# Performance work log

Measured on AMD Instinct MI355X. Metric: run time of the kernel, lower is better.

## Reference

```python
import jax, jax.numpy as jnp
import numpy as np

EPS = 0.1
P, C, T_MLP, C_MLP, B = 196, 768, 384, 3072, 64


def yat(x, W, b, alpha):
    # x: (..., in), W: (out, in), b: (out,), alpha: (1,)
    dot_nb = jnp.einsum('...i,oi->...o', x, W)          # no-bias dot (shared GEMM)
    dot = dot_nb + b
    w_norm_sq = jnp.sum(W * W, axis=1)                   # (out,)
    x_norm_sq = jnp.sum(x * x, axis=-1, keepdims=True)   # (..., 1)
    dist_sq = w_norm_sq + x_norm_sq - 2.0 * dot_nb
    out_f = W.shape[0]
    scale_base = out_f / np.log(out_f + 1.0)
    scale = jnp.sqrt(jnp.asarray(scale_base, x.dtype)) ** alpha[0]
    return scale * (dot * dot) / (dist_sq + EPS)


def setup_inputs() -> dict:
    key = jax.random.key(0)
    ks = jax.random.split(key, 7)
    x = jax.random.normal(ks[0], (B, P, C), dtype=jnp.float32)
    # token-mixing YAT: in=P, out=T_MLP
    tw = jax.random.normal(ks[1], (T_MLP, P), dtype=jnp.float32) / np.sqrt(P)
    tb = jnp.zeros((T_MLP,), jnp.float32)
    t_alpha = jnp.ones((1,), jnp.float32)
    # token-mixing linear: T_MLP -> P
    w2 = jax.random.uniform(ks[2], (P, T_MLP), jnp.float32, -1, 1) / np.sqrt(T_MLP)
    b2 = jax.random.uniform(ks[3], (P,), jnp.float32, -1, 1) / np.sqrt(T_MLP)
    # channel-mixing YAT: in=C, out=C_MLP
    cw = jax.random.normal(ks[4], (C_MLP, C), dtype=jnp.float32) / np.sqrt(C)
    cb = jnp.zeros((C_MLP,), jnp.float32)
    c_alpha = jnp.ones((1,), jnp.float32)
    # channel-mixing linear: C_MLP -> C
    w4 = jax.random.uniform(ks[5], (C, C_MLP), jnp.float32, -1, 1) / np.sqrt(C_MLP)
    b4 = jax.random.uniform(ks[6], (C,), jnp.float32, -1, 1) / np.sqrt(C_MLP)
    return {"x": x, "tw": tw, "tb": tb, "t_alpha": t_alpha, "w2": w2, "b2": b2,
            "cw": cw, "cb": cb, "c_alpha": c_alpha, "w4": w4, "b4": b4}


def reference(x, tw, tb, t_alpha, w2, b2, cw, cb, c_alpha, w4, b4):
    # Token mixing (operates over patch dim)
    shortcut = x
    xt = jnp.swapaxes(x, 1, 2)                 # (B, C, P)
    h = yat(xt, tw, tb, t_alpha)               # (B, C, T_MLP)
    h = jnp.einsum('bct,pt->bcp', h, w2) + b2  # (B, C, P)
    x = shortcut + jnp.swapaxes(h, 1, 2)
    # Channel mixing (operates over hidden dim)
    shortcut = x
    h = yat(x, cw, cb, c_alpha)                # (B, P, C_MLP)
    h = jnp.einsum('bpm,cm->bpc', h, w4) + b4  # (B, P, C)
    return shortcut + h
```

## Files before the change

### kernel.cpp

```cpp
#include <hip/hip_runtime.h>
#include <hip/hip_bf16.h>
#include <math.h>

#define B_   64
#define P_   196
#define PPAD 224
#define C_   768
#define TM_  384
#define CM_  3072
#define EPSY 0.1f

typedef unsigned short u16;
typedef __attribute__((ext_vector_type(8))) short bf16x8;
typedef __attribute__((ext_vector_type(4))) float f32x4;

__device__ __forceinline__ float bf2f(u16 v) {
    return __uint_as_float(((unsigned int)v) << 16);
}
__device__ __forceinline__ u16 f2bf(float f) {
    unsigned int u = __float_as_uint(f);
    unsigned int rounding = 0x7FFFu + ((u >> 16) & 1u);
    return (u16)((u + rounding) >> 16);
}

__device__ __forceinline__ void gl_lds16(const u16* g, u16* l) {
    __builtin_amdgcn_global_load_lds(
        (const __attribute__((address_space(1))) unsigned int*)g,
        (__attribute__((address_space(3))) unsigned int*)l,
        16, 0, 0);
}


__global__ __launch_bounds__(256) void k_prep_xT(const float* __restrict__ x,
                                                 u16* __restrict__ xT,
                                                 float* __restrict__ xn1) {
    __shared__ u16 tile[32][33];
    __shared__ float colsum[32];
    const int b = blockIdx.z, p0 = blockIdx.x * 32, c0 = blockIdx.y * 32;
    const int tx = threadIdx.x & 31, ty = threadIdx.x >> 5;
    if (threadIdx.x < 32) colsum[threadIdx.x] = 0.f;
    const float* xb = x + (size_t)b * P_ * C_;
    float s = 0.f;
    #pragma unroll
    for (int r = 0; r < 4; ++r) {
        int p = p0 + ty + r * 8;
        float v = (p < P_) ? xb[(size_t)p * C_ + c0 + tx] : 0.f;
        u16 h = f2bf(v);
        tile[ty + r * 8][tx] = h;
        float vb = bf2f(h);
        s = fmaf(vb, vb, s);
    }
    __syncthreads();
    u16* dst = xT + ((size_t)b * C_ + c0) * PPAD + p0;
    #pragma unroll
    for (int r = 0; r < 4; ++r) {
        int cl = ty + r * 8;
        dst[(size_t)cl * PPAD + tx] = tile[tx][cl];
    }
    atomicAdd(&colsum[tx], s);
    __syncthreads();
    if (threadIdx.x < 32)
        atomicAdd(&xn1[(size_t)b * C_ + c0 + threadIdx.x], colsum[threadIdx.x]);
}

__device__ __forceinline__ void pad_norm_body(const float* in, u16* outb, float* norm,
                                              int rows, int inlen, int outlen,
                                              int bid, int tid) {
    int wave = (bid * 256 + tid) >> 6;
    int lane = tid & 63;
    if (wave >= rows) return;
    const float* src = in + (size_t)wave * inlen;
    u16* dst = outb + (size_t)wave * outlen;
    float s = 0.f;
    for (int i = lane; i < outlen; i += 64) {
        float v = (i < inlen) ? src[i] : 0.f;
        u16 h = f2bf(v);
        dst[i] = h;
        float vv = bf2f(h);
        s = fmaf(vv, vv, s);
    }
    #pragma unroll
    for (int off = 32; off > 0; off >>= 1) s += __shfl_down(s, off, 64);
    if (lane == 0) norm[wave] = s;
}

__global__ __launch_bounds__(256) void k_prep_weights(
    const float* __restrict__ tw, u16* __restrict__ twb, float* __restrict__ twn,
    const float* __restrict__ cw, u16* __restrict__ cwb, float* __restrict__ cwn,
    const float* __restrict__ w2, u16* __restrict__ w2b,
    const float* __restrict__ w4, u16* __restrict__ w4b) {
    int bid = blockIdx.x, tid = threadIdx.x;
    if (bid < 96) {
        pad_norm_body(tw, twb, twn, TM_, P_, PPAD, bid, tid);
    } else if (bid < 864) {
        pad_norm_body(cw, cwb, cwn, CM_, C_, C_, bid - 96, tid);
    } else if (bid < 1248) {
        int idx = (bid - 864) * 256 + tid;
        int row = idx / TM_;
        w2b[idx] = (row < P_) ? f2bf(w2[(size_t)row * TM_ + (idx % TM_)]) : (u16)0;
    } else {
        int idx = (bid - 1248) * 256 + tid;
        float4 v = ((const float4*)w4)[idx];
        ushort4 o;
        o.x = f2bf(v.x); o.y = f2bf(v.y); o.z = f2bf(v.z); o.w = f2bf(v.w);
        ((ushort4*)w4b)[idx] = o;
    }
}

__device__ __forceinline__ void mfma_mainloop(
    const u16* __restrict__ A, const u16* __restrict__ B,
    int lda, int ldb, int kiters,
    f32x4 (&acc)[4][4], u16* As, u16* Bs) {
    const int t = threadIdx.x;
    const int wid = t >> 6, lane = t & 63;
    const int quad = lane >> 4, l15 = lane & 15;
    const u16* Aw = As + (wid >> 1) * (64 * 32);
    const u16* Bw = Bs + (wid & 1) * (64 * 32);
    const int row0 = t >> 2, kc = (t & 3) * 8;
    const int row1 = 64 + row0;

    for (int it = 0; it < kiters; ++it) {
        int k0 = it * 32;
        gl_lds16(A + (size_t)row0 * lda + k0 + kc, As + wid * 512);
        gl_lds16(A + (size_t)row1 * lda + k0 + kc, As + 2048 + wid * 512);
        gl_lds16(B + (size_t)row0 * ldb + k0 + kc, Bs + wid * 512);
        gl_lds16(B + (size_t)row1 * ldb + k0 + kc, Bs + 2048 + wid * 512);
        __syncthreads();
        bf16x8 af[4], bfr[4];
        #pragma unroll
        for (int i = 0; i < 4; ++i)
            af[i] = *(const bf16x8*)(Aw + ((i * 16 + l15) * 32 + quad * 8));
        #pragma unroll
        for (int j = 0; j < 4; ++j)
            bfr[j] = *(const bf16x8*)(Bw + ((j * 16 + l15) * 32 + quad * 8));
        #pragma unroll
        for (int i = 0; i < 4; ++i)
            #pragma unroll
            for (int j = 0; j < 4; ++j)
                acc[i][j] = __builtin_amdgcn_mfma_f32_16x16x32_bf16(af[i], bfr[j], acc[i][j], 0, 0, 0);
        __syncthreads();
    }
}

#define MFMA_PROLOGUE(AP, BP, LDA, LDB, KITERS)                          \
    __shared__ u16 As[128 * 32];                                         \
    __shared__ u16 Bs[128 * 32];                                         \
    const int t = threadIdx.x;                                           \
    const int wid = t >> 6, lane = t & 63;                               \
    const int quad = lane >> 4, l15 = lane & 15;                         \
    const int m0 = blockIdx.x * 128, n0 = blockIdx.y * 128;              \
    f32x4 acc[4][4];                                                     \
    _Pragma("unroll")                                                    \
    for (int i = 0; i < 4; ++i)                                          \
        _Pragma("unroll")                                                \
        for (int j = 0; j < 4; ++j) acc[i][j] = (f32x4){0.f,0.f,0.f,0.f};\
    mfma_mainloop(AP, BP, LDA, LDB, KITERS, acc, As, Bs);                \
    const int rbase = m0 + (wid >> 1) * 64;                              \
    const int cbase = n0 + (wid & 1) * 64;

__global__ __launch_bounds__(256) void k1_token_yat(
    const u16* __restrict__ xT, const u16* __restrict__ twb,
    const float* __restrict__ tb, const float* __restrict__ twn,
    const float* __restrict__ xn1, const float* __restrict__ alpha, float sb,
    u16* __restrict__ h1) {
    MFMA_PROLOGUE(xT + (size_t)m0 * PPAD, twb + (size_t)n0 * PPAD, PPAD, PPAD, PPAD / 32)
    float scale = powf(sqrtf(sb), alpha[0]);
    #pragma unroll
    for (int i = 0; i < 4; ++i) {
        #pragma unroll
        for (int j = 0; j < 4; ++j) {
            int col = cbase + j * 16 + l15;
            float bn = tb[col], wnn = twn[col];
            #pragma unroll
            for (int reg = 0; reg < 4; ++reg) {
                int row = rbase + i * 16 + quad * 4 + reg;
                float dnb = acc[i][j][reg];
                float dot = dnb + bn;
                float dist = wnn + xn1[row] - 2.f * dnb;
                h1[(size_t)row * TM_ + col] = f2bf(scale * dot * dot / (dist + EPSY));
            }
        }
    }
}

__global__ __launch_bounds__(256) void k3_chan_yat(
    const u16* __restrict__ x1b, const u16* __restrict__ cwb,
    const float* __restrict__ cb, const float* __restrict__ cwn,
    const float* __restrict__ xn2, const float* __restrict__ alpha, float sb,
    u16* __restrict__ h3) {
    MFMA_PROLOGUE(x1b + (size_t)m0 * C_, cwb + (size_t)n0 * C_, C_, C_, C_ / 32)
    float scale = powf(sqrtf(sb), alpha[0]);
    #pragma unroll
    for (int i = 0; i < 4; ++i) {
        #pragma unroll
        for (int j = 0; j < 4; ++j) {
            int col = cbase + j * 16 + l15;
            float bn = cb[col], wnn = cwn[col];
            #pragma unroll
            for (int reg = 0; reg < 4; ++reg) {
                int row = rbase + i * 16 + quad * 4 + reg;
                float dnb = acc[i][j][reg];
                float dot = dnb + bn;
                float dist = wnn + xn2[row] - 2.f * dnb;
                h3[(size_t)row * CM_ + col] = f2bf(scale * dot * dot / (dist + EPSY));
            }
        }
    }
}

__global__ __launch_bounds__(256) void k2_token_out(
    const u16* __restrict__ w2b, const u16* __restrict__ h1,
    const float* __restrict__ b2, const float* __restrict__ x,
    float* __restrict__ xn2, u16* __restrict__ x1b) {
    const u16* Bz = h1 + (size_t)blockIdx.z * C_ * TM_;
    MFMA_PROLOGUE(w2b + (size_t)m0 * TM_, Bz + (size_t)n0 * TM_, TM_, TM_, TM_ / 32)
    const float* rz = x + (size_t)blockIdx.z * P_ * C_;
    u16* oz = x1b + (size_t)blockIdx.z * P_ * C_;
    float* xrow = xn2 + (size_t)blockIdx.z * P_;
    #pragma unroll
    for (int i = 0; i < 4; ++i) {
        #pragma unroll
        for (int reg = 0; reg < 4; ++reg) {
            int row = rbase + i * 16 + quad * 4 + reg;
            if (row < P_) {
                float bm = b2[row];
                float s = 0.f;
                #pragma unroll
                for (int j = 0; j < 4; ++j) {
                    int col = cbase + j * 16 + l15;
                    float v = acc[i][j][reg] + bm + rz[(size_t)row * C_ + col];
                    u16 h = f2bf(v);
                    oz[(size_t)row * C_ + col] = h;
                    float vb = bf2f(h);
                    s = fmaf(vb, vb, s);
                }
                s += __shfl_xor(s, 1, 64);
                s += __shfl_xor(s, 2, 64);
                s += __shfl_xor(s, 4, 64);
                s += __shfl_xor(s, 8, 64);
                if (l15 == 0) atomicAdd(&xrow[row], s);
            }
        }
    }
}

__global__ __launch_bounds__(256) void k4_split(
    const u16* __restrict__ h3, const u16* __restrict__ w4b,
    float* __restrict__ outp, float* __restrict__ pbuf, int KK) {
    const int kbase = blockIdx.z * KK;
    MFMA_PROLOGUE(h3 + (size_t)m0 * CM_ + kbase, w4b + (size_t)n0 * CM_ + kbase,
                  CM_, CM_, KK / 32)
    float* dst = (blockIdx.z == 0) ? outp
               : pbuf + (size_t)(blockIdx.z - 1) * ((size_t)B_ * P_ * C_);
    #pragma unroll
    for (int i = 0; i < 4; ++i) {
        #pragma unroll
        for (int j = 0; j < 4; ++j) {
            int col = cbase + j * 16 + l15;
            #pragma unroll
            for (int reg = 0; reg < 4; ++reg) {
                int row = rbase + i * 16 + quad * 4 + reg;
                dst[(size_t)row * C_ + col] = acc[i][j][reg];
            }
        }
    }
}

template <int NS>
__global__ __launch_bounds__(256) void k4_reduce(
    float* __restrict__ outp, const float* __restrict__ pbuf,
    const u16* __restrict__ x1b, const float* __restrict__ b4) {
    int idx = blockIdx.x * 256 + threadIdx.x;
    int c = (idx * 4) % C_;
    float4 o = ((const float4*)outp)[idx];
    const size_t stride4 = (size_t)B_ * P_ * C_ / 4;
    #pragma unroll
    for (int s = 0; s < NS - 1; ++s) {
        float4 p = ((const float4*)pbuf)[idx + s * stride4];
        o.x += p.x; o.y += p.y; o.z += p.z; o.w += p.w;
    }
    ushort4 r = ((const ushort4*)x1b)[idx];
    o.x += bf2f(r.x) + b4[c + 0];
    o.y += bf2f(r.y) + b4[c + 1];
    o.z += bf2f(r.z) + b4[c + 2];
    o.w += bf2f(r.w) + b4[c + 3];
    ((float4*)outp)[idx] = o;
}

__global__ __launch_bounds__(256) void gemm_k4_fb(
    const u16* __restrict__ A, const u16* __restrict__ Bmat,
    const float* __restrict__ biasN, const u16* __restrict__ resB,
    float* __restrict__ Fout) {
    __shared__ u16 As[128 * 32];
    __shared__ u16 Bs[64 * 32];
    const int t = threadIdx.x;
    const int wid = t >> 6, lane = t & 63;
    const int quad = lane >> 4, l15 = lane & 15;
    const int m0 = blockIdx.x * 128, n0 = blockIdx.y * 64;
    f32x4 acc[4][2];
    #pragma unroll
    for (int i = 0; i < 4; ++i)
        #pragma unroll
        for (int j = 0; j < 2; ++j) acc[i][j] = (f32x4){0.f, 0.f, 0.f, 0.f};
    const u16* Aw = As + (wid >> 1) * (64 * 32);
    const u16* Bw = Bs + (wid & 1) * (32 * 32);
    const int arow = t >> 2, akc = (t & 3) * 8;
    for (int k0 = 0; k0 < CM_; k0 += 32) {
        gl_lds16(A + (size_t)(m0 + arow) * CM_ + k0 + akc,      As + wid * 512);
        gl_lds16(A + (size_t)(m0 + 64 + arow) * CM_ + k0 + akc, As + 2048 + wid * 512);
        gl_lds16(Bmat + (size_t)(n0 + arow) * CM_ + k0 + akc,   Bs + wid * 512);
        __syncthreads();
        bf16x8 af[4], bfr[2];
        #pragma unroll
        for (int i = 0; i < 4; ++i)
            af[i] = *(const bf16x8*)(Aw + ((i * 16 + l15) * 32 + quad * 8));
        #pragma unroll
        for (int j = 0; j < 2; ++j)
            bfr[j] = *(const bf16x8*)(Bw + ((j * 16 + l15) * 32 + quad * 8));
        #pragma unroll
        for (int i = 0; i < 4; ++i)
            #pragma unroll
            for (int j = 0; j < 2; ++j)
                acc[i][j] = __builtin_amdgcn_mfma_f32_16x16x32_bf16(af[i], bfr[j], acc[i][j], 0, 0, 0);
        __syncthreads();
    }
    const int rbase = m0 + (wid >> 1) * 64;
    const int cbase = n0 + (wid & 1) * 32;
    #pragma unroll
    for (int i = 0; i < 4; ++i) {
        #pragma unroll
        for (int j = 0; j < 2; ++j) {
            int col = cbase + j * 16 + l15;
            float bn = biasN[col];
            #pragma unroll
            for (int reg = 0; reg < 4; ++reg) {
                int row = rbase + i * 16 + quad * 4 + reg;
                float v = acc[i][j][reg] + bn + bf2f(resB[(size_t)row * C_ + col]);
                Fout[(size_t)row * C_ + col] = v;
            }
        }
    }
}

extern "C" void kernel_launch(void* const* d_in, const int* in_sizes, int n_in,
                              void* d_out, int out_size, void* d_ws, size_t ws_size,
                              hipStream_t stream) {
    const float* x  = (const float*)d_in[0];
    const float* tw = (const float*)d_in[1];
    const float* tb = (const float*)d_in[2];
    const float* ta = (const float*)d_in[3];
    const float* w2 = (const float*)d_in[4];
    const float* b2 = (const float*)d_in[5];
    const float* cw = (const float*)d_in[6];
    const float* cb = (const float*)d_in[7];
    const float* ca = (const float*)d_in[8];
    const float* w4 = (const float*)d_in[9];
    const float* b4 = (const float*)d_in[10];
    float* out = (float*)d_out;

    char* ws = (char*)d_ws;
    u16* h1 = (u16*)ws;
    u16* xT = (u16*)(ws + 37748736);
    u16* h3 = (u16*)ws;
    size_t off = 77070336;
    u16* x1b = (u16*)(ws + off); off += (size_t)B_ * P_ * C_ * 2;
    u16* twb = (u16*)(ws + off); off += (size_t)TM_ * PPAD * 2;
    u16* w2b = (u16*)(ws + off); off += (size_t)256 * TM_ * 2;
    u16* cwb = (u16*)(ws + off); off += (size_t)CM_ * C_ * 2;
    u16* w4b = (u16*)(ws + off); off += (size_t)C_ * CM_ * 2;
    float* xn1 = (float*)(ws + off); off += (size_t)B_ * C_ * 4;
    float* xn2 = (float*)(ws + off); off += (size_t)B_ * P_ * 4;
    float* twn = (float*)(ws + off); off += (size_t)TM_ * 4;
    float* cwn = (float*)(ws + off); off += (size_t)CM_ * 4;
    float* pbuf = (float*)(ws + off);
    const size_t psz = (size_t)B_ * P_ * C_ * 4;

    int nsplit = 1;
    if (ws_size >= off + 3 * psz)      nsplit = 4;
    else if (ws_size >= off + psz)     nsplit = 2;

    const float SBT = (float)TM_ / logf((float)TM_ + 1.0f);
    const float SBC = (float)CM_ / logf((float)CM_ + 1.0f);

    hipMemsetAsync(xn1, 0, (size_t)(B_ * C_ + B_ * P_) * 4, stream);
    k_prep_weights<<<3552, 256, 0, stream>>>(tw, twb, twn, cw, cwb, cwn,
                                             w2, w2b, w4, w4b);
    k_prep_xT<<<dim3(PPAD / 32, C_ / 32, B_), 256, 0, stream>>>(x, xT, xn1);

    k1_token_yat<<<dim3(B_ * C_ / 128, TM_ / 128), 256, 0, stream>>>(
        xT, twb, tb, twn, xn1, ta, SBT, h1);

    k2_token_out<<<dim3(2, C_ / 128, B_), 256, 0, stream>>>(
        w2b, h1, b2, x, xn2, x1b);

    k3_chan_yat<<<dim3(B_ * P_ / 128, CM_ / 128), 256, 0, stream>>>(
        x1b, cwb, cb, cwn, xn2, ca, SBC, h3);

    if (nsplit > 1) {
        k4_split<<<dim3(B_ * P_ / 128, C_ / 128, nsplit), 256, 0, stream>>>(
            h3, w4b, out, pbuf, CM_ / nsplit);
        int n4 = B_ * P_ * C_ / 4;
        if (nsplit == 4)
            k4_reduce<4><<<(n4 + 255) / 256, 256, 0, stream>>>(out, pbuf, x1b, b4);
        else
            k4_reduce<2><<<(n4 + 255) / 256, 256, 0, stream>>>(out, pbuf, x1b, b4);
    } else {
        gemm_k4_fb<<<dim3(B_ * P_ / 128, C_ / 64), 256, 0, stream>>>(
            h3, w4b, b4, x1b, out);
    }
}
```

Before: 441.7 us.

## Double K-tile depth to 64 with XOR-swizzled LDS layout in MFMA GEMMs

The shared MFMA mainloop now stages a 128x64 K-slab per iteration instead of 128x32, halving the number of barrier pairs per GEMM and issuing more direct-to-LDS loads per sync. The LDS layout uses an XOR swizzle on 16-byte chunks to avoid bank conflicts on the fragment reads. The token-mixing padding grows from 224 to 256 so the K loop divides by 64, which adds extra zero-padded work in the token YAT GEMM. LDS use per block doubles, which may lower occupancy.

```diff
diff --git a/kernel.cpp b/kernel.cpp
--- a/kernel.cpp
+++ b/kernel.cpp
@@ -4,7 +4,7 @@
 
 #define B_   64
 #define P_   196
-#define PPAD 224
+#define PPAD 256
 #define C_   768
 #define TM_  384
 #define CM_  3072
@@ -107,44 +107,52 @@
     }
 }
 
-__device__ __forceinline__ void mfma_mainloop(
+__device__ __forceinline__ void mfma_mainloop64(
     const u16* __restrict__ A, const u16* __restrict__ B,
     int lda, int ldb, int kiters,
     f32x4 (&acc)[4][4], u16* As, u16* Bs) {
     const int t = threadIdx.x;
-    const int wid = t >> 6, lane = t & 63;
-    const int quad = lane >> 4, l15 = lane & 15;
-    const u16* Aw = As + (wid >> 1) * (64 * 32);
-    const u16* Bw = Bs + (wid & 1) * (64 * 32);
-    const int row0 = t >> 2, kc = (t & 3) * 8;
-    const int row1 = 64 + row0;
+    const int w = t >> 6, l = t & 63;
+    const int quad = l >> 4, l15 = l & 15;
+    const int srow = w * 32 + (l >> 3);
+    const int scol = ((l & 7) ^ (l >> 3)) * 8;
+    u16* dstA = As + w * 2048 + l * 8;
+    u16* dstB = Bs + w * 2048 + l * 8;
+    const int arow = (w >> 1) * 64 + l15;
+    const int brow = (w & 1) * 64 + l15;
+    const int sw = (l15 & 7);
 
     for (int it = 0; it < kiters; ++it) {
-        int k0 = it * 32;
-        gl_lds16(A + (size_t)row0 * lda + k0 + kc, As + wid * 512);
-        gl_lds16(A + (size_t)row1 * lda + k0 + kc, As + 2048 + wid * 512);
-        gl_lds16(B + (size_t)row0 * ldb + k0 + kc, Bs + wid * 512);
-        gl_lds16(B + (size_t)row1 * ldb + k0 + kc, Bs + 2048 + wid * 512);
+        const int k0 = it * 64;
+        #pragma unroll
+        for (int u = 0; u < 4; ++u) {
+            gl_lds16(A + (size_t)(srow + u * 8) * lda + k0 + scol, dstA + u * 512);
+            gl_lds16(B + (size_t)(srow + u * 8) * ldb + k0 + scol, dstB + u * 512);
+        }
         __syncthreads();
-        bf16x8 af[4], bfr[4];
-        #pragma unroll
-        for (int i = 0; i < 4; ++i)
-            af[i] = *(const bf16x8*)(Aw + ((i * 16 + l15) * 32 + quad * 8));
-        #pragma unroll
-        for (int j = 0; j < 4; ++j)
-            bfr[j] = *(const bf16x8*)(Bw + ((j * 16 + l15) * 32 + quad * 8));
-        #pragma unroll
-        for (int i = 0; i < 4; ++i)
+        #pragma unroll
+        for (int h = 0; h < 2; ++h) {
+            const int kx = ((quad + h * 4) ^ sw) * 8;
+            bf16x8 af[4], bfr[4];
+            #pragma unroll
+            for (int i = 0; i < 4; ++i)
+                af[i] = *(const bf16x8*)(As + (arow + i * 16) * 64 + kx);
             #pragma unroll
             for (int j = 0; j < 4; ++j)
-                acc[i][j] = __builtin_amdgcn_mfma_f32_16x16x32_bf16(af[i], bfr[j], acc[i][j], 0, 0, 0);
+                bfr[j] = *(const bf16x8*)(Bs + (brow + j * 16) * 64 + kx);
+            #pragma unroll
+            for (int i = 0; i < 4; ++i)
+                #pragma unroll
+                for (int j = 0; j < 4; ++j)
+                    acc[i][j] = __builtin_amdgcn_mfma_f32_16x16x32_bf16(af[i], bfr[j], acc[i][j], 0, 0, 0);
+        }
         __syncthreads();
     }
 }
 
-#define MFMA_PROLOGUE(AP, BP, LDA, LDB, KITERS)                          \
-    __shared__ u16 As[128 * 32];                                         \
-    __shared__ u16 Bs[128 * 32];                                         \
+#define MFMA_PROLOGUE64(AP, BP, LDA, LDB, KITERS)                        \
+    __shared__ u16 As[128 * 64];                                         \
+    __shared__ u16 Bs[128 * 64];                                         \
     const int t = threadIdx.x;                                           \
     const int wid = t >> 6, lane = t & 63;                               \
     const int quad = lane >> 4, l15 = lane & 15;                         \
@@ -154,7 +162,7 @@
     for (int i = 0; i < 4; ++i)                                          \
         _Pragma("unroll")                                                \
         for (int j = 0; j < 4; ++j) acc[i][j] = (f32x4){0.f,0.f,0.f,0.f};\
-    mfma_mainloop(AP, BP, LDA, LDB, KITERS, acc, As, Bs);                \
+    mfma_mainloop64(AP, BP, LDA, LDB, KITERS, acc, As, Bs);              \
     const int rbase = m0 + (wid >> 1) * 64;                              \
     const int cbase = n0 + (wid & 1) * 64;
 
@@ -163,7 +171,7 @@
     const float* __restrict__ tb, const float* __restrict__ twn,
     const float* __restrict__ xn1, const float* __restrict__ alpha, float sb,
     u16* __restrict__ h1) {
-    MFMA_PROLOGUE(xT + (size_t)m0 * PPAD, twb + (size_t)n0 * PPAD, PPAD, PPAD, PPAD / 32)
+    MFMA_PROLOGUE64(xT + (size_t)m0 * PPAD, twb + (size_t)n0 * PPAD, PPAD, PPAD, PPAD / 64)
     float scale = powf(sqrtf(sb), alpha[0]);
     #pragma unroll
     for (int i = 0; i < 4; ++i) {
@@ -188,7 +196,7 @@
     const float* __restrict__ cb, const float* __restrict__ cwn,
     const float* __restrict__ xn2, const float* __restrict__ alpha, float sb,
     u16* __restrict__ h3) {
-    MFMA_PROLOGUE(x1b + (size_t)m0 * C_, cwb + (size_t)n0 * C_, C_, C_, C_ / 32)
+    MFMA_PROLOGUE64(x1b + (size_t)m0 * C_, cwb + (size_t)n0 * C_, C_, C_, C_ / 64)
     float scale = powf(sqrtf(sb), alpha[0]);
     #pragma unroll
     for (int i = 0; i < 4; ++i) {
@@ -213,7 +221,7 @@
     const float* __restrict__ b2, const float* __restrict__ x,
     float* __restrict__ xn2, u16* __restrict__ x1b) {
     const u16* Bz = h1 + (size_t)blockIdx.z * C_ * TM_;
-    MFMA_PROLOGUE(w2b + (size_t)m0 * TM_, Bz + (size_t)n0 * TM_, TM_, TM_, TM_ / 32)
+    MFMA_PROLOGUE64(w2b + (size_t)m0 * TM_, Bz + (size_t)n0 * TM_, TM_, TM_, TM_ / 64)
     const float* rz = x + (size_t)blockIdx.z * P_ * C_;
     u16* oz = x1b + (size_t)blockIdx.z * P_ * C_;
     float* xrow = xn2 + (size_t)blockIdx.z * P_;
@@ -248,8 +256,8 @@
     const u16* __restrict__ h3, const u16* __restrict__ w4b,
     float* __restrict__ outp, float* __restrict__ pbuf, int KK) {
     const int kbase = blockIdx.z * KK;
-    MFMA_PROLOGUE(h3 + (size_t)m0 * CM_ + kbase, w4b + (size_t)n0 * CM_ + kbase,
-                  CM_, CM_, KK / 32)
+    MFMA_PROLOGUE64(h3 + (size_t)m0 * CM_ + kbase, w4b + (size_t)n0 * CM_ + kbase,
+                    CM_, CM_, KK / 64)
     float* dst = (blockIdx.z == 0) ? outp
                : pbuf + (size_t)(blockIdx.z - 1) * ((size_t)B_ * P_ * C_);
     #pragma unroll
@@ -287,6 +295,7 @@
     ((float4*)outp)[idx] = o;
 }
 
+__device__ __forceinline__ void gl_lds16_fb(const u16* g, u16* l) { gl_lds16(g, l); }
 __global__ __launch_bounds__(256) void gemm_k4_fb(
     const u16* __restrict__ A, const u16* __restrict__ Bmat,
     const float* __restrict__ biasN, const u16* __restrict__ resB,
@@ -306,9 +315,9 @@
     const u16* Bw = Bs + (wid & 1) * (32 * 32);
     const int arow = t >> 2, akc = (t & 3) * 8;
     for (int k0 = 0; k0 < CM_; k0 += 32) {
-        gl_lds16(A + (size_t)(m0 + arow) * CM_ + k0 + akc,      As + wid * 512);
-        gl_lds16(A + (size_t)(m0 + 64 + arow) * CM_ + k0 + akc, As + 2048 + wid * 512);
-        gl_lds16(Bmat + (size_t)(n0 + arow) * CM_ + k0 + akc,   Bs + wid * 512);
+        gl_lds16_fb(A + (size_t)(m0 + arow) * CM_ + k0 + akc,      As + wid * 512);
+        gl_lds16_fb(A + (size_t)(m0 + 64 + arow) * CM_ + k0 + akc, As + 2048 + wid * 512);
+        gl_lds16_fb(Bmat + (size_t)(n0 + arow) * CM_ + k0 + akc,   Bs + wid * 512);
         __syncthreads();
         bf16x8 af[4], bfr[2];
         #pragma unroll
```

Result: slower. 465.4 us (+5.4%).

## Reorder GEMM grids for weight-tile locality and store split-K partials as bf16

Applied to the files above, without the earlier changes.

The k1, k3 and k4 grids are remapped so the N (weight) tile comes from blockIdx.z and M tiles are spread across x/y. Consecutive blocks therefore share the same weight tile, which should improve L2 reuse. k3 and k4 gain a guard for the padded M range. The split-K partials in k4 are now written as bf16 into a separate buffer for every split, including the first one that used to go straight to the output. The reduce kernel starts from the residual plus bias and adds all bf16 partials, which halves partial traffic but loses some precision in the partial sums.

```diff
diff --git a/kernel.cpp b/kernel.cpp
--- a/kernel.cpp
+++ b/kernel.cpp
@@ -112,19 +112,19 @@
     int lda, int ldb, int kiters,
     f32x4 (&acc)[4][4], u16* As, u16* Bs) {
     const int t = threadIdx.x;
-    const int wid = t >> 6, lane = t & 63;
-    const int quad = lane >> 4, l15 = lane & 15;
-    const u16* Aw = As + (wid >> 1) * (64 * 32);
-    const u16* Bw = Bs + (wid & 1) * (64 * 32);
+    const int w = t >> 6, l = t & 63;
+    const int quad = l >> 4, l15 = l & 15;
+    const u16* Aw = As + (w >> 1) * (64 * 32);
+    const u16* Bw = Bs + (w & 1) * (64 * 32);
     const int row0 = t >> 2, kc = (t & 3) * 8;
     const int row1 = 64 + row0;
 
     for (int it = 0; it < kiters; ++it) {
         int k0 = it * 32;
-        gl_lds16(A + (size_t)row0 * lda + k0 + kc, As + wid * 512);
-        gl_lds16(A + (size_t)row1 * lda + k0 + kc, As + 2048 + wid * 512);
-        gl_lds16(B + (size_t)row0 * ldb + k0 + kc, Bs + wid * 512);
-        gl_lds16(B + (size_t)row1 * ldb + k0 + kc, Bs + 2048 + wid * 512);
+        gl_lds16(A + (size_t)row0 * lda + k0 + kc, As + w * 512);
+        gl_lds16(A + (size_t)row1 * lda + k0 + kc, As + 2048 + w * 512);
+        gl_lds16(B + (size_t)row0 * ldb + k0 + kc, Bs + w * 512);
+        gl_lds16(B + (size_t)row1 * ldb + k0 + kc, Bs + 2048 + w * 512);
         __syncthreads();
         bf16x8 af[4], bfr[4];
         #pragma unroll
@@ -142,13 +142,12 @@
     }
 }
 
-#define MFMA_PROLOGUE(AP, BP, LDA, LDB, KITERS)                          \
+#define MFMA_CORE(AP, BP, LDA, LDB, KITERS)                              \
     __shared__ u16 As[128 * 32];                                         \
     __shared__ u16 Bs[128 * 32];                                         \
     const int t = threadIdx.x;                                           \
     const int wid = t >> 6, lane = t & 63;                               \
     const int quad = lane >> 4, l15 = lane & 15;                         \
-    const int m0 = blockIdx.x * 128, n0 = blockIdx.y * 128;              \
     f32x4 acc[4][4];                                                     \
     _Pragma("unroll")                                                    \
     for (int i = 0; i < 4; ++i)                                          \
@@ -163,7 +162,9 @@
     const float* __restrict__ tb, const float* __restrict__ twn,
     const float* __restrict__ xn1, const float* __restrict__ alpha, float sb,
     u16* __restrict__ h1) {
-    MFMA_PROLOGUE(xT + (size_t)m0 * PPAD, twb + (size_t)n0 * PPAD, PPAD, PPAD, PPAD / 32)
+    const int m0 = (blockIdx.x + blockIdx.y * 8) * 128;
+    const int n0 = blockIdx.z * 128;
+    MFMA_CORE(xT + (size_t)m0 * PPAD, twb + (size_t)n0 * PPAD, PPAD, PPAD, PPAD / 32)
     float scale = powf(sqrtf(sb), alpha[0]);
     #pragma unroll
     for (int i = 0; i < 4; ++i) {
@@ -188,7 +189,11 @@
     const float* __restrict__ cb, const float* __restrict__ cwn,
     const float* __restrict__ xn2, const float* __restrict__ alpha, float sb,
     u16* __restrict__ h3) {
-    MFMA_PROLOGUE(x1b + (size_t)m0 * C_, cwb + (size_t)n0 * C_, C_, C_, C_ / 32)
+    const int mt = blockIdx.x + blockIdx.y * 8;
+    if (mt >= B_ * P_ / 128) return;
+    const int m0 = mt * 128;
+    const int n0 = blockIdx.z * 128;
+    MFMA_CORE(x1b + (size_t)m0 * C_, cwb + (size_t)n0 * C_, C_, C_, C_ / 32)
     float scale = powf(sqrtf(sb), alpha[0]);
     #pragma unroll
     for (int i = 0; i < 4; ++i) {
@@ -212,8 +217,9 @@
     const u16* __restrict__ w2b, const u16* __restrict__ h1,
     const float* __restrict__ b2, const float* __restrict__ x,
     float* __restrict__ xn2, u16* __restrict__ x1b) {
+    const int m0 = blockIdx.x * 128, n0 = blockIdx.y * 128;
     const u16* Bz = h1 + (size_t)blockIdx.z * C_ * TM_;
-    MFMA_PROLOGUE(w2b + (size_t)m0 * TM_, Bz + (size_t)n0 * TM_, TM_, TM_, TM_ / 32)
+    MFMA_CORE(w2b + (size_t)m0 * TM_, Bz + (size_t)n0 * TM_, TM_, TM_, TM_ / 32)
     const float* rz = x + (size_t)blockIdx.z * P_ * C_;
     u16* oz = x1b + (size_t)blockIdx.z * P_ * C_;
     float* xrow = xn2 + (size_t)blockIdx.z * P_;
@@ -246,12 +252,17 @@
 
 __global__ __launch_bounds__(256) void k4_split(
     const u16* __restrict__ h3, const u16* __restrict__ w4b,
-    float* __restrict__ outp, float* __restrict__ pbuf, int KK) {
-    const int kbase = blockIdx.z * KK;
-    MFMA_PROLOGUE(h3 + (size_t)m0 * CM_ + kbase, w4b + (size_t)n0 * CM_ + kbase,
-                  CM_, CM_, KK / 32)
-    float* dst = (blockIdx.z == 0) ? outp
-               : pbuf + (size_t)(blockIdx.z - 1) * ((size_t)B_ * P_ * C_);
+    u16* __restrict__ pbuf, int KK) {
+    const int mt = blockIdx.x + blockIdx.y * 8;
+    if (mt >= B_ * P_ / 128) return;
+    const int m0 = mt * 128;
+    const int nz = blockIdx.z;
+    const int n0 = (nz % (C_ / 128)) * 128;
+    const int ks = nz / (C_ / 128);
+    const int kbase = ks * KK;
+    MFMA_CORE(h3 + (size_t)m0 * CM_ + kbase, w4b + (size_t)n0 * CM_ + kbase,
+              CM_, CM_, KK / 32)
+    u16* dst = pbuf + (size_t)ks * ((size_t)B_ * P_ * C_);
     #pragma unroll
     for (int i = 0; i < 4; ++i) {
         #pragma unroll
@@ -260,7 +271,7 @@
             #pragma unroll
             for (int reg = 0; reg < 4; ++reg) {
                 int row = rbase + i * 16 + quad * 4 + reg;
-                dst[(size_t)row * C_ + col] = acc[i][j][reg];
+                dst[(size_t)row * C_ + col] = f2bf(acc[i][j][reg]);
             }
         }
     }
@@ -268,22 +279,22 @@
 
 template <int NS>
 __global__ __launch_bounds__(256) void k4_reduce(
-    float* __restrict__ outp, const float* __restrict__ pbuf,
+    float* __restrict__ outp, const u16* __restrict__ pbuf,
     const u16* __restrict__ x1b, const float* __restrict__ b4) {
     int idx = blockIdx.x * 256 + threadIdx.x;
     int c = (idx * 4) % C_;
-    float4 o = ((const float4*)outp)[idx];
+    ushort4 r = ((const ushort4*)x1b)[idx];
+    float4 o;
+    o.x = bf2f(r.x) + b4[c + 0];
+    o.y = bf2f(r.y) + b4[c + 1];
+    o.z = bf2f(r.z) + b4[c + 2];
+    o.w = bf2f(r.w) + b4[c + 3];
     const size_t stride4 = (size_t)B_ * P_ * C_ / 4;
     #pragma unroll
-    for (int s = 0; s < NS - 1; ++s) {
-        float4 p = ((const float4*)pbuf)[idx + s * stride4];
-        o.x += p.x; o.y += p.y; o.z += p.z; o.w += p.w;
-    }
-    ushort4 r = ((const ushort4*)x1b)[idx];
-    o.x += bf2f(r.x) + b4[c + 0];
-    o.y += bf2f(r.y) + b4[c + 1];
-    o.z += bf2f(r.z) + b4[c + 2];
-    o.w += bf2f(r.w) + b4[c + 3];
+    for (int s = 0; s < NS; ++s) {
+        ushort4 p = ((const ushort4*)pbuf)[idx + s * stride4];
+        o.x += bf2f(p.x); o.y += bf2f(p.y); o.z += bf2f(p.z); o.w += bf2f(p.w);
+    }
     ((float4*)outp)[idx] = o;
 }
 
@@ -372,12 +383,12 @@
     float* xn2 = (float*)(ws + off); off += (size_t)B_ * P_ * 4;
     float* twn = (float*)(ws + off); off += (size_t)TM_ * 4;
     float* cwn = (float*)(ws + off); off += (size_t)CM_ * 4;
-    float* pbuf = (float*)(ws + off);
-    const size_t psz = (size_t)B_ * P_ * C_ * 4;
+    u16* pbuf = (u16*)(ws + off);
+    const size_t psz = (size_t)B_ * P_ * C_ * 2;
 
     int nsplit = 1;
-    if (ws_size >= off + 3 * psz)      nsplit = 4;
-    else if (ws_size >= off + psz)     nsplit = 2;
+    if (ws_size >= off + 4 * psz)      nsplit = 4;
+    else if (ws_size >= off + 2 * psz) nsplit = 2;
 
     const float SBT = (float)TM_ / logf((float)TM_ + 1.0f);
     const float SBC = (float)CM_ / logf((float)CM_ + 1.0f);
@@ -387,18 +398,18 @@
                                              w2, w2b, w4, w4b);
     k_prep_xT<<<dim3(PPAD / 32, C_ / 32, B_), 256, 0, stream>>>(x, xT, xn1);
 
-    k1_token_yat<<<dim3(B_ * C_ / 128, TM_ / 128), 256, 0, stream>>>(
+    k1_token_yat<<<dim3(8, 48, 3), 256, 0, stream>>>(
         xT, twb, tb, twn, xn1, ta, SBT, h1);
 
     k2_token_out<<<dim3(2, C_ / 128, B_), 256, 0, stream>>>(
         w2b, h1, b2, x, xn2, x1b);
 
-    k3_chan_yat<<<dim3(B_ * P_ / 128, CM_ / 128), 256, 0, stream>>>(
+    k3_chan_yat<<<dim3(8, 13, 24), 256, 0, stream>>>(
         x1b, cwb, cb, cwn, xn2, ca, SBC, h3);
 
     if (nsplit > 1) {
-        k4_split<<<dim3(B_ * P_ / 128, C_ / 128, nsplit), 256, 0, stream>>>(
-            h3, w4b, out, pbuf, CM_ / nsplit);
+        k4_split<<<dim3(8, 13, (C_ / 128) * nsplit), 256, 0, stream>>>(
+            h3, w4b, pbuf, CM_ / nsplit);
         int n4 = B_ * P_ * C_ / 4;
         if (nsplit == 4)
             k4_reduce<4><<<(n4 + 255) / 256, 256, 0, stream>>>(out, pbuf, x1b, b4);
```

Measured after the change: 421.8 us. 1.05x faster.
